# Performance work log

Measured on AMD Instinct MI355X. Metric: run time of the kernel, lower is better.

Reference implementation:

```python
import jax, jax.numpy as jnp
import numpy as np

T = 32.0                       # softmax temperature
THRESH = float(np.cos(np.pi * 40.0 / 180.0))  # cos(degree), degree=40
NEG_INF = -9.0e15


def setup_inputs() -> dict:
    key = jax.random.key(0)
    ks = jax.random.split(key, 11)
    B, C, D_IMG, D_ATT, H_ATT, H = 2048, 1000, 2048, 312, 128, 128
    def rn(k, shape, scale=1.0):
        return jax.random.normal(k, shape, dtype=jnp.float32) * scale
    return {
        "image_feats": rn(ks[0], (B, D_IMG)),
        "img_proto":   rn(ks[1], (C, D_IMG)),
        "attributes":  rn(ks[2], (C, D_ATT)),
        "unused":      0,
        # parameters
        "att_g":   rn(ks[3], (D_ATT, H_ATT), 0.05),
        "slim_w":  rn(ks[4], (D_IMG, D_ATT), 0.02),   # proto_slim weight (transposed torch layout)
        "slim_b":  rn(ks[5], (D_ATT,), 0.02),
        "img_w":   rn(ks[6], (D_IMG, H), 0.02),
        "proto_w": rn(ks[7], (2 * D_ATT, H), 0.02),   # att_dim + proto_red_dim = 624
        "proto_b": rn(ks[8], (1, H), 0.02),
        "fc_w":    rn(ks[9], (H, 1), 0.05),
        "fc_b":    rn(ks[10], (1,), 0.05),
    }


def reference(image_feats, img_proto, attributes, unused,
              att_g, slim_w, slim_b, img_w, proto_w, proto_b, fc_w, fc_b):
    # proto_slim: [C, D_img] -> [C, att_dim]
    proto_red = img_proto @ slim_w + slim_b

    # --- get_attention: cosine similarity among attribute projections ---
    g = attributes @ att_g                                   # [C, att_hC] (g == h in original)
    gn = g / jnp.clip(jnp.linalg.norm(g, axis=1, keepdims=True), 1e-12)
    sim = gn @ gn.T                                          # [C, C] cosine similarity
    raw = jnp.where(sim > THRESH, sim, NEG_INF)              # threshold mask
    attn = jax.nn.softmax(raw * T, axis=1)                   # [C, C]

    # --- propagate prototypes ---
    att_outs = attn @ attributes                             # [C, att_dim]
    img_proto_outs = attn @ proto_red                        # [C, att_dim]
    outs = jnp.concatenate([att_outs, img_proto_outs], axis=1)  # [C, 2*att_dim]

    # --- relation MLP (broadcast instead of materialized expand+matmul) ---
    img_h = image_feats @ img_w                              # [B, H]
    proto_h = outs @ proto_w                                 # [C, H]
    hidden = jax.nn.relu(img_h[:, None, :] + proto_h[None, :, :] + proto_b)  # [B, C, H]
    outputs = hidden @ fc_w + fc_b                           # [B, C, 1]
    return outputs[..., 0]                                   # [B, C]
```

## Files before the change

### kernel.cpp

```cpp
#include <hip/hip_runtime.h>

typedef unsigned short ushort_t;
typedef __bf16 bf16x8 __attribute__((ext_vector_type(8)));
typedef float f32x4 __attribute__((ext_vector_type(4)));
typedef float f32x2 __attribute__((ext_vector_type(2)));
typedef ushort_t us4 __attribute__((ext_vector_type(4)));

#define T_SOFT 32.0f
#define THRESH 0.76604444311897803f
#define SW 1048

__device__ __forceinline__ ushort_t f2bf(float f) {
  union { float f; unsigned u; } x; x.f = f;
  unsigned r = (x.u + 0x7fffu + ((x.u >> 16) & 1u)) >> 16;
  return (ushort_t)r;
}
__device__ __forceinline__ float bf2f(ushort_t h) {
  union { unsigned u; float f; } x; x.u = ((unsigned)h) << 16; return x.f;
}

__device__ __forceinline__ us4 pack4(float4 x) {
  union { unsigned u[2]; us4 h; } r;
  union { float4 f; unsigned u[4]; } a;
  a.f = x;
  r.u[0] = __builtin_amdgcn_perm(a.u[1] + 0x8000u, a.u[0] + 0x8000u, 0x07060302u);
  r.u[1] = __builtin_amdgcn_perm(a.u[3] + 0x8000u, a.u[2] + 0x8000u, 0x07060302u);
  return r.h;
}

__global__ __launch_bounds__(256) void tr3_k(const float* __restrict__ s0, ushort_t* __restrict__ d0,
                                             const float* __restrict__ s1, ushort_t* __restrict__ d1,
                                             const float* __restrict__ s2, ushort_t* __restrict__ d2,
                                             const float* __restrict__ attributes, ushort_t* __restrict__ poutN,
                                             ushort_t* __restrict__ gn_bf, float* __restrict__ zero_base) {
  int b = blockIdx.x, tid = threadIdx.x;
  if (b >= 976) {
    if (b < 1288) {
      int t = (b - 976) * 256 + tid;
      int row = t / 78, c4 = (t - row * 78) * 4;
      us4 v = {0, 0, 0, 0};
      if (row < 1000) v = pack4(*reinterpret_cast<const float4*>(attributes + (size_t)row * 312 + c4));
      *reinterpret_cast<us4*>(poutN + (size_t)row * 640 + c4) = v;
    } else if (b < 1432) {
      int t = (b - 1288) * 256 + tid;
      float4* zp = reinterpret_cast<float4*>(zero_base) + (size_t)t * 4;
      float4 z = make_float4(0.f, 0.f, 0.f, 0.f);
      zp[0] = z; zp[1] = z; zp[2] = z; zp[3] = z;
    } else {
      us4 z = {0, 0, 0, 0};
      *reinterpret_cast<us4*>(gn_bf + 1000 * 128 + tid * 4) = z;
    }
    return;
  }
  __shared__ float tl[32][33];
  const float* src; ushort_t* dst; int R, C, Cw, Rpad, local, ctiles;
  if (b < 640)       { src = s0; dst = d0; R = 2048; C = 312; Cw = 320; Rpad = 2048; local = b;       ctiles = 10; }
  else if (b < 896)  { src = s1; dst = d1; R = 2048; C = 128; Cw = 128; Rpad = 2048; local = b - 640; ctiles = 4;  }
  else               { src = s2; dst = d2; R = 624;  C = 128; Cw = 128; Rpad = 640;  local = b - 896; ctiles = 4;  }
  int rt = local / ctiles, ct = local - rt * ctiles;
  int r0 = rt * 32, c0 = ct * 32;
  #pragma unroll
  for (int p = 0; p < 4; ++p) {
    int idx = p * 256 + tid;
    int rr = idx >> 5, cc = idx & 31;
    float v = 0.f;
    if (r0 + rr < R && c0 + cc < C) v = src[(size_t)(r0 + rr) * C + (c0 + cc)];
    tl[cc][rr] = v;
  }
  __syncthreads();
  int cc = tid >> 3, rq = tid & 7;
  if (c0 + cc < Cw) {
    us4 o;
    o[0] = f2bf(tl[cc][rq * 4 + 0]);
    o[1] = f2bf(tl[cc][rq * 4 + 1]);
    o[2] = f2bf(tl[cc][rq * 4 + 2]);
    o[3] = f2bf(tl[cc][rq * 4 + 3]);
    *reinterpret_cast<us4*>(dst + (size_t)(c0 + cc) * Rpad + r0 + rq * 4) = o;
  }
}

__device__ __forceinline__ void gemm_imgh(const float* __restrict__ A, const ushort_t* __restrict__ BT,
                                          float* __restrict__ C, int r0, int k0,
                                          ushort_t* __restrict__ As, ushort_t* __restrict__ Bs, int tid) {
  const int SA = 72;
  int lane = tid & 63, wv = tid >> 6;
  int l15 = lane & 15, quad = lane >> 4;
  int arow = tid >> 4, akq = tid & 15;
  int brow = tid >> 3, bkq = tid & 7;
  const float* agp[8];
  #pragma unroll
  for (int p = 0; p < 8; ++p) agp[p] = A + (size_t)(r0 + arow + p * 16) * 2048 + k0 + akq * 4;
  const ushort_t* bgp[4];
  #pragma unroll
  for (int p = 0; p < 4; ++p) bgp[p] = BT + (size_t)(brow + p * 32) * 2048 + k0 + bkq * 8;

  float4 ap[8]; bf16x8 bp[4];
  #pragma unroll
  for (int p = 0; p < 8; ++p) ap[p] = *reinterpret_cast<const float4*>(agp[p]);
  #pragma unroll
  for (int p = 0; p < 4; ++p) bp[p] = *reinterpret_cast<const bf16x8*>(bgp[p]);

  f32x4 acc[2][8];
  #pragma unroll
  for (int i = 0; i < 2; ++i)
    #pragma unroll
    for (int j = 0; j < 8; ++j) acc[i][j] = f32x4{0.f, 0.f, 0.f, 0.f};

  for (int s = 0; s < 4; ++s) {
    if (s) __syncthreads();
    #pragma unroll
    for (int p = 0; p < 8; ++p)
      *reinterpret_cast<us4*>(As + (arow + p * 16) * SA + akq * 4) = pack4(ap[p]);
    #pragma unroll
    for (int p = 0; p < 4; ++p)
      *reinterpret_cast<bf16x8*>(Bs + (brow + p * 32) * SA + bkq * 8) = bp[p];
    if (s + 1 < 4) {
      #pragma unroll
      for (int p = 0; p < 8; ++p) ap[p] = *reinterpret_cast<const float4*>(agp[p] + 64);
      #pragma unroll
      for (int p = 0; p < 4; ++p) bp[p] = *reinterpret_cast<const bf16x8*>(bgp[p] + 64);
      #pragma unroll
      for (int p = 0; p < 8; ++p) agp[p] += 64;
      #pragma unroll
      for (int p = 0; p < 4; ++p) bgp[p] += 64;
    }
    __syncthreads();
    #pragma unroll
    for (int kh = 0; kh < 2; ++kh) {
      bf16x8 af[2];
      #pragma unroll
      for (int pi = 0; pi < 2; ++pi)
        af[pi] = *reinterpret_cast<bf16x8*>(As + ((wv * 2 + pi) * 16 + l15) * SA + kh * 32 + quad * 8);
      #pragma unroll
      for (int ct = 0; ct < 8; ++ct) {
        bf16x8 bfr = *reinterpret_cast<bf16x8*>(Bs + (ct * 16 + l15) * SA + kh * 32 + quad * 8);
        acc[0][ct] = __builtin_amdgcn_mfma_f32_16x16x32_bf16(af[0], bfr, acc[0][ct], 0, 0, 0);
        acc[1][ct] = __builtin_amdgcn_mfma_f32_16x16x32_bf16(af[1], bfr, acc[1][ct], 0, 0, 0);
      }
    }
  }
  #pragma unroll
  for (int pi = 0; pi < 2; ++pi)
    #pragma unroll
    for (int ct = 0; ct < 8; ++ct) {
      int col = ct * 16 + l15;
      #pragma unroll
      for (int r = 0; r < 4; ++r) {
        int row = r0 + (wv * 2 + pi) * 16 + quad * 4 + r;
        atomicAdd(&C[(size_t)row * 128 + col], acc[pi][ct][r]);
      }
    }
}

__device__ __forceinline__ void gemm_proto(const float* __restrict__ A, const ushort_t* __restrict__ BT,
                                           float* __restrict__ pacc2, int r0, int c0, int k0,
                                           ushort_t* __restrict__ As, ushort_t* __restrict__ Bs, int tid) {
  const int SA = 72;
  int lane = tid & 63, wv = tid >> 6;
  int l15 = lane & 15, quad = lane >> 4;
  int arow = tid >> 4, akq = tid & 15;
  int brow = tid >> 3, bkq = tid & 7;
  const float* agp[8];
  #pragma unroll
  for (int p = 0; p < 8; ++p) {
    int r = r0 + arow + p * 16; if (r >= 1000) r = 999;
    agp[p] = A + (size_t)r * 2048 + k0 + akq * 4;
  }
  const ushort_t* bgp[4];
  #pragma unroll
  for (int p = 0; p < 4; ++p) {
    int n = c0 + brow + p * 32; if (n >= 320) n = 319;
    bgp[p] = BT + (size_t)n * 2048 + k0 + bkq * 8;
  }
  float4 ap[8]; bf16x8 bp[4];
  #pragma unroll
  for (int p = 0; p < 8; ++p) ap[p] = *reinterpret_cast<const float4*>(agp[p]);
  #pragma unroll
  for (int p = 0; p < 4; ++p) bp[p] = *reinterpret_cast<const bf16x8*>(bgp[p]);

  f32x4 acc[2][8];
  #pragma unroll
  for (int i = 0; i < 2; ++i)
    #pragma unroll
    for (int j = 0; j < 8; ++j) acc[i][j] = f32x4{0.f, 0.f, 0.f, 0.f};

  for (int s = 0; s < 4; ++s) {
    if (s) __syncthreads();
    #pragma unroll
    for (int p = 0; p < 8; ++p)
      *reinterpret_cast<us4*>(As + (arow + p * 16) * SA + akq * 4) = pack4(ap[p]);
    #pragma unroll
    for (int p = 0; p < 4; ++p)
      *reinterpret_cast<bf16x8*>(Bs + (brow + p * 32) * SA + bkq * 8) = bp[p];
    if (s + 1 < 4) {
      #pragma unroll
      for (int p = 0; p < 8; ++p) ap[p] = *reinterpret_cast<const float4*>(agp[p] + 64);
      #pragma unroll
      for (int p = 0; p < 4; ++p) bp[p] = *reinterpret_cast<const bf16x8*>(bgp[p] + 64);
      #pragma unroll
      for (int p = 0; p < 8; ++p) agp[p] += 64;
      #pragma unroll
      for (int p = 0; p < 4; ++p) bgp[p] += 64;
    }
    __syncthreads();
    #pragma unroll
    for (int kh = 0; kh < 2; ++kh) {
      bf16x8 af[2];
      #pragma unroll
      for (int pi = 0; pi < 2; ++pi)
        af[pi] = *reinterpret_cast<bf16x8*>(As + ((wv * 2 + pi) * 16 + l15) * SA + kh * 32 + quad * 8);
      #pragma unroll
      for (int ct = 0; ct < 8; ++ct) {
        bf16x8 bfr = *reinterpret_cast<bf16x8*>(Bs + (ct * 16 + l15) * SA + kh * 32 + quad * 8);
        acc[0][ct] = __builtin_amdgcn_mfma_f32_16x16x32_bf16(af[0], bfr, acc[0][ct], 0, 0, 0);
        acc[1][ct] = __builtin_amdgcn_mfma_f32_16x16x32_bf16(af[1], bfr, acc[1][ct], 0, 0, 0);
      }
    }
  }
  #pragma unroll
  for (int pi = 0; pi < 2; ++pi)
    #pragma unroll
    for (int ct = 0; ct < 8; ++ct) {
      int col = c0 + ct * 16 + l15;
      if (col < 320) {
        #pragma unroll
        for (int r = 0; r < 4; ++r) {
          int row = r0 + (wv * 2 + pi) * 16 + quad * 4 + r;
          atomicAdd(&pacc2[(size_t)row * 320 + col], acc[pi][ct][r]);
        }
      }
    }
}

__global__ __launch_bounds__(256) void mega_k(
    const float* __restrict__ attributes, const float* __restrict__ att_g,
    ushort_t* __restrict__ gn_bf,
    const float* __restrict__ img_proto, const ushort_t* __restrict__ slimT,
    const float* __restrict__ image_feats, const ushort_t* __restrict__ imgwT,
    float* __restrict__ img_h, float* __restrict__ pacc2) {
  __shared__ ushort_t As[128 * 72];
  __shared__ ushort_t Bs[128 * 72];
  int b = blockIdx.x, tid = threadIdx.x;
  if (b < 125) {
    __shared__ float a_lds[8][316];
    __shared__ float red2[8][2];
    int h = tid & 127;
    int c0 = b * 8;
    for (int idx = tid; idx < 8 * 312; idx += 256) {
      int r = idx / 312;
      int k = idx - r * 312;
      a_lds[r][k] = attributes[(c0 + r) * 312 + k];
    }
    __syncthreads();
    float acc[8] = {0.f,0.f,0.f,0.f,0.f,0.f,0.f,0.f};
    for (int k = 0; k < 312; k += 4) {
      float w0 = att_g[(k + 0) * 128 + h];
      float w1 = att_g[(k + 1) * 128 + h];
      float w2 = att_g[(k + 2) * 128 + h];
      float w3 = att_g[(k + 3) * 128 + h];
      #pragma unroll
      for (int r = 0; r < 8; ++r) {
        float4 a4 = *reinterpret_cast<const float4*>(&a_lds[r][k]);
        acc[r] += a4.x * w0 + a4.y * w1 + a4.z * w2 + a4.w * w3;
      }
    }
    int lane = tid & 63, wvid = (tid >> 6) & 1;
    #pragma unroll
    for (int r = 0; r < 8; ++r) {
      float v = acc[r] * acc[r];
      #pragma unroll
      for (int off = 32; off > 0; off >>= 1) v += __shfl_xor(v, off, 64);
      if (lane == 0) red2[r][wvid] = v;
    }
    __syncthreads();
    #pragma unroll
    for (int r = 0; r < 8; ++r) {
      float nrm = fmaxf(sqrtf(red2[r][0] + red2[r][1]), 1e-12f);
      gn_bf[(c0 + r) * 128 + h] = f2bf(acc[r] / nrm);
    }
    return;
  }
  b -= 125;
  if (b < 128) {
    int tile = b >> 3, kc = b & 7;
    gemm_imgh(image_feats, imgwT, img_h, tile * 128, kc * 256, As, Bs, tid);
  } else {
    b -= 128;
    int tile = b >> 3, kc = b & 7;
    int rb = tile / 3, cb = tile - rb * 3;
    gemm_proto(img_proto, slimT, pacc2, rb * 128, cb * 128, kc * 256, As, Bs, tid);
  }
}

__global__ __launch_bounds__(256) void conv_k(const float* __restrict__ pacc2, ushort_t* __restrict__ poutN) {
  int t = blockIdx.x * 256 + threadIdx.x;
  int row = t / 82, m = (t - row * 82) * 4;
  us4 v = {0, 0, 0, 0};
  if (m < 320) v = pack4(*reinterpret_cast<const float4*>(pacc2 + (size_t)row * 320 + m));
  *reinterpret_cast<us4*>(poutN + (size_t)row * 640 + 312 + m) = v;
}

__global__ __launch_bounds__(256) void g_k(const ushort_t* __restrict__ protowT, const ushort_t* __restrict__ poutN,
                                           const float* __restrict__ proto_w, const float* __restrict__ slim_b,
                                           const float* __restrict__ proto_b,
                                           ushort_t* __restrict__ GT, float* __restrict__ biasG) {
  int b = blockIdx.x, tid = threadIdx.x;
  if (b >= 8) {
    int h = tid & 127;
    float acc = proto_b[h];
    for (int n = 0; n < 312; n += 4) {
      acc += slim_b[n + 0] * proto_w[(size_t)(312 + n) * 128 + h];
      acc += slim_b[n + 1] * proto_w[(size_t)(313 + n) * 128 + h];
      acc += slim_b[n + 2] * proto_w[(size_t)(314 + n) * 128 + h];
      acc += slim_b[n + 3] * proto_w[(size_t)(315 + n) * 128 + h];
    }
    if (tid < 128) biasG[h] = acc;
    return;
  }
  const int SA = 72;
  __shared__ ushort_t As[128 * 72];
  __shared__ ushort_t Bs[128 * 72];
  int lane = tid & 63, wv = tid >> 6;
  int l15 = lane & 15, quad = lane >> 4;
  int hrow = tid >> 3, hkq = tid & 7;
  size_t j0 = (size_t)b * 128;
  const ushort_t* agp[4];
  const ushort_t* bgp[4];
  #pragma unroll
  for (int p = 0; p < 4; ++p) {
    agp[p] = protowT + (size_t)(hrow + p * 32) * 640 + hkq * 8;
    bgp[p] = poutN + (j0 + hrow + p * 32) * 640 + hkq * 8;
  }
  bf16x8 ar[4], br[4];
  #pragma unroll
  for (int p = 0; p < 4; ++p) { ar[p] = *reinterpret_cast<const bf16x8*>(agp[p]); br[p] = *reinterpret_cast<const bf16x8*>(bgp[p]); }

  f32x4 acc[2][8];
  #pragma unroll
  for (int i = 0; i < 2; ++i)
    #pragma unroll
    for (int j = 0; j < 8; ++j) acc[i][j] = f32x4{0.f, 0.f, 0.f, 0.f};

  for (int s = 0; s < 10; ++s) {
    if (s) __syncthreads();
    #pragma unroll
    for (int p = 0; p < 4; ++p) {
      *reinterpret_cast<bf16x8*>(As + (hrow + p * 32) * SA + hkq * 8) = ar[p];
      *reinterpret_cast<bf16x8*>(Bs + (hrow + p * 32) * SA + hkq * 8) = br[p];
    }
    if (s + 1 < 10) {
      #pragma unroll
      for (int p = 0; p < 4; ++p) {
        ar[p] = *reinterpret_cast<const bf16x8*>(agp[p] + 64);
        br[p] = *reinterpret_cast<const bf16x8*>(bgp[p] + 64);
        agp[p] += 64; bgp[p] += 64;
      }
    }
    __syncthreads();
    #pragma unroll
    for (int kh = 0; kh < 2; ++kh) {
      bf16x8 af[2];
      #pragma unroll
      for (int pi = 0; pi < 2; ++pi)
        af[pi] = *reinterpret_cast<bf16x8*>(As + ((wv * 2 + pi) * 16 + l15) * SA + kh * 32 + quad * 8);
      #pragma unroll
      for (int ct = 0; ct < 8; ++ct) {
        bf16x8 bfr = *reinterpret_cast<bf16x8*>(Bs + (ct * 16 + l15) * SA + kh * 32 + quad * 8);
        acc[0][ct] = __builtin_amdgcn_mfma_f32_16x16x32_bf16(af[0], bfr, acc[0][ct], 0, 0, 0);
        acc[1][ct] = __builtin_amdgcn_mfma_f32_16x16x32_bf16(af[1], bfr, acc[1][ct], 0, 0, 0);
      }
    }
  }
  #pragma unroll
  for (int pi = 0; pi < 2; ++pi)
    #pragma unroll
    for (int ct = 0; ct < 8; ++ct) {
      int col = ct * 16 + l15;
      #pragma unroll
      for (int r = 0; r < 4; ++r) {
        int row = (wv * 2 + pi) * 16 + quad * 4 + r;
        GT[(size_t)row * 1024 + j0 + col] = f2bf(acc[pi][ct][r]);
      }
    }
}

__global__ __launch_bounds__(256) void attn5_k(
    const ushort_t* __restrict__ gn_bf, const ushort_t* __restrict__ GT,
    const float* __restrict__ biasG, float* __restrict__ ph) {
  __shared__ ushort_t W[16 * SW];
  __shared__ float rsum[16];
  __shared__ int flags[63];
  int tid = threadIdx.x;
  int i0 = blockIdx.x * 16;
  int lane = tid & 63, wv = tid >> 6;
  int l15 = lane & 15, quad = lane >> 4;
  if (tid < 63) flags[tid] = 0;
  if (tid >= 64 && tid < 80) rsum[tid - 64] = 0.f;
  W[(tid >> 4) * SW + 1008 + (tid & 15)] = 0;
  __syncthreads();

  const ushort_t* abase = gn_bf + (size_t)(i0 + l15) * 128 + quad * 8;
  bf16x8 af0 = *reinterpret_cast<const bf16x8*>(abase);
  bf16x8 af1 = *reinterpret_cast<const bf16x8*>(abase + 32);
  bf16x8 af2 = *reinterpret_cast<const bf16x8*>(abase + 64);
  bf16x8 af3 = *reinterpret_cast<const bf16x8*>(abase + 96);
  float rs[4] = {0.f, 0.f, 0.f, 0.f};
  for (int jt = wv; jt < 63; jt += 4) {
    const ushort_t* bbase = gn_bf + (size_t)(jt * 16 + l15) * 128 + quad * 8;
    f32x4 d = {0.f, 0.f, 0.f, 0.f};
    d = __builtin_amdgcn_mfma_f32_16x16x32_bf16(af0, *reinterpret_cast<const bf16x8*>(bbase),      d, 0, 0, 0);
    d = __builtin_amdgcn_mfma_f32_16x16x32_bf16(af1, *reinterpret_cast<const bf16x8*>(bbase + 32), d, 0, 0, 0);
    d = __builtin_amdgcn_mfma_f32_16x16x32_bf16(af2, *reinterpret_cast<const bf16x8*>(bbase + 64), d, 0, 0, 0);
    d = __builtin_amdgcn_mfma_f32_16x16x32_bf16(af3, *reinterpret_cast<const bf16x8*>(bbase + 96), d, 0, 0, 0);
    int hot = 0;
    #pragma unroll
    for (int r = 0; r < 4; ++r) {
      float w = 0.f;
      if (d[r] > THRESH) { w = __expf(T_SOFT * (d[r] - 1.0f)); hot = 1; }
      ushort_t wb = f2bf(w);
      W[(quad * 4 + r) * SW + jt * 16 + l15] = wb;
      rs[r] += bf2f(wb);
    }
    if (hot) flags[jt] = 1;
  }
  #pragma unroll
  for (int r = 0; r < 4; ++r) {
    float v = rs[r];
    v += __shfl_xor(v, 1, 64); v += __shfl_xor(v, 2, 64);
    v += __shfl_xor(v, 4, 64); v += __shfl_xor(v, 8, 64);
    if (l15 == 0) atomicAdd(&rsum[quad * 4 + r], v);
  }
  __syncthreads();

  f32x4 acc2[2];
  acc2[0] = f32x4{0.f, 0.f, 0.f, 0.f};
  acc2[1] = f32x4{0.f, 0.f, 0.f, 0.f};
  for (int s = 0; s < 32; ++s) {
    int f = flags[2 * s] | ((2 * s + 1 < 63) ? flags[2 * s + 1] : 0);
    if (!f) continue;
    bf16x8 a = *reinterpret_cast<bf16x8*>(W + l15 * SW + s * 32 + quad * 8);
    #pragma unroll
    for (int t = 0; t < 2; ++t) {
      int h = (wv * 2 + t) * 16 + l15;
      bf16x8 bfr = *reinterpret_cast<const bf16x8*>(GT + (size_t)h * 1024 + s * 32 + quad * 8);
      acc2[t] = __builtin_amdgcn_mfma_f32_16x16x32_bf16(a, bfr, acc2[t], 0, 0, 0);
    }
  }
  #pragma unroll
  for (int t = 0; t < 2; ++t) {
    int h = (wv * 2 + t) * 16 + l15;
    float bg = biasG[h];
    #pragma unroll
    for (int r = 0; r < 4; ++r) {
      int row = quad * 4 + r;
      int gi = i0 + row;
      float inv = 1.f / fmaxf(rsum[row], 1e-30f);
      if (gi < 1000) ph[(size_t)gi * 128 + h] = acc2[t][r] * inv + bg;
    }
  }
}

__global__ __launch_bounds__(512) void final_k(
    const float* __restrict__ img_h, const float* __restrict__ ph,
    const float* __restrict__ fc_w, const float* __restrict__ fc_b,
    float* __restrict__ out) {
  __shared__ float ih[128][132];
  __shared__ float ps[64][132];
  __shared__ float ws_[128];
  int tid = threadIdx.x;
  int b0 = blockIdx.x * 128;
  int c0 = blockIdx.y * 64;
  for (int idx = tid; idx < 4096; idx += 512) {
    int row = idx >> 5, c4 = (idx & 31) * 4;
    float4 v = *reinterpret_cast<const float4*>(img_h + (size_t)(b0 + row) * 128 + c4);
    *reinterpret_cast<float4*>(&ih[row][c4]) = v;
  }
  for (int idx = tid; idx < 2048; idx += 512) {
    int row = idx >> 5, c4 = (idx & 31) * 4;
    int c = c0 + row;
    float4 v = make_float4(0.f, 0.f, 0.f, 0.f);
    if (c < 1000) v = *reinterpret_cast<const float4*>(ph + (size_t)c * 128 + c4);
    *reinterpret_cast<float4*>(&ps[row][c4]) = v;
  }
  if (tid < 128) ws_[tid] = fc_w[tid];
  __syncthreads();
  int tx = tid & 15, ty = tid >> 4;
  f32x2 acc[4][4] = {};
  const f32x2 zero2 = {0.f, 0.f};
  for (int h = 0; h < 128; h += 4) {
    float4 w4 = *reinterpret_cast<float4*>(&ws_[h]);
    f32x2 wlo = {w4.x, w4.y}, whi = {w4.z, w4.w};
    float4 a4[4], p4[4];
    #pragma unroll
    for (int i = 0; i < 4; ++i) a4[i] = *reinterpret_cast<float4*>(&ih[ty * 4 + i][h]);
    #pragma unroll
    for (int j = 0; j < 4; ++j) p4[j] = *reinterpret_cast<float4*>(&ps[tx * 4 + j][h]);
    #pragma unroll
    for (int i = 0; i < 4; ++i) {
      f32x2 alo = {a4[i].x, a4[i].y}, ahi = {a4[i].z, a4[i].w};
      #pragma unroll
      for (int j = 0; j < 4; ++j) {
        f32x2 plo = {p4[j].x, p4[j].y}, phi = {p4[j].z, p4[j].w};
        f32x2 t0 = __builtin_elementwise_max(alo + plo, zero2);
        f32x2 t1 = __builtin_elementwise_max(ahi + phi, zero2);
        acc[i][j] = acc[i][j] + t0 * wlo;
        acc[i][j] = acc[i][j] + t1 * whi;
      }
    }
  }
  float fb = fc_b[0];
  #pragma unroll
  for (int i = 0; i < 4; ++i) {
    int b = b0 + ty * 4 + i;
    int c = c0 + tx * 4;
    if (c < 1000) {
      float4 v = make_float4(acc[i][0].x + acc[i][0].y + fb, acc[i][1].x + acc[i][1].y + fb,
                             acc[i][2].x + acc[i][2].y + fb, acc[i][3].x + acc[i][3].y + fb);
      *reinterpret_cast<float4*>(out + (size_t)b * 1000 + c) = v;
    }
  }
}

extern "C" void kernel_launch(void* const* d_in, const int* in_sizes, int n_in,
                              void* d_out, int out_size, void* d_ws, size_t ws_size,
                              hipStream_t stream) {
  const float* image_feats = (const float*)d_in[0];
  const float* img_proto   = (const float*)d_in[1];
  const float* attributes  = (const float*)d_in[2];
  const float* att_g   = (const float*)d_in[4];
  const float* slim_w  = (const float*)d_in[5];
  const float* slim_b  = (const float*)d_in[6];
  const float* img_w   = (const float*)d_in[7];
  const float* proto_w = (const float*)d_in[8];
  const float* proto_b = (const float*)d_in[9];
  const float* fc_w    = (const float*)d_in[10];
  const float* fc_b    = (const float*)d_in[11];
  float* out = (float*)d_out;

  char* ws = (char*)d_ws;
  size_t o = 0;
  auto alloc = [&](size_t bytes) { size_t r = o; o += (bytes + 255) & ~(size_t)255; return r; };
  ushort_t* imgwT   = (ushort_t*)(ws + alloc(128ull * 2048 * 2));
  ushort_t* slimT   = (ushort_t*)(ws + alloc(320ull * 2048 * 2));
  ushort_t* protowT = (ushort_t*)(ws + alloc(128ull * 640 * 2));
  ushort_t* gn_bf   = (ushort_t*)(ws + alloc(1008ull * 128 * 2));
  ushort_t* poutN   = (ushort_t*)(ws + alloc(1024ull * 640 * 2));
  ushort_t* GT      = (ushort_t*)(ws + alloc(128ull * 1024 * 2));
  float* biasG     = (float*)(ws + alloc(128ull * 4));
  float* img_h     = (float*)(ws + alloc(2048ull * 128 * 4));
  float* pacc2     = (float*)(ws + alloc(1024ull * 320 * 4));
  float* ph        = (float*)(ws + alloc(1000ull * 128 * 4));

  tr3_k<<<1433, 256, 0, stream>>>(slim_w, slimT, img_w, imgwT, proto_w, protowT,
                                  attributes, poutN, gn_bf, img_h);

  mega_k<<<445, 256, 0, stream>>>(attributes, att_g, gn_bf,
                                  img_proto, slimT,
                                  image_feats, imgwT, img_h, pacc2);

  conv_k<<<328, 256, 0, stream>>>(pacc2, poutN);

  g_k<<<9, 256, 0, stream>>>(protowT, poutN, proto_w, slim_b, proto_b, GT, biasG);

  attn5_k<<<63, 256, 0, stream>>>(gn_bf, GT, biasG, ph);

  final_k<<<dim3(16, 16), 512, 0, stream>>>(img_h, ph, fc_w, fc_b, out);
}
```

Before: 179.3 us.

## Reassociate proto path to fold slim_w into proto_w and drop atomics

```diff
diff --git a/kernel.cpp b/kernel.cpp
--- a/kernel.cpp
+++ b/kernel.cpp
@@ -28,36 +28,56 @@
   return r.h;
 }
 
-__global__ __launch_bounds__(256) void tr3_k(const float* __restrict__ s0, ushort_t* __restrict__ d0,
-                                             const float* __restrict__ s1, ushort_t* __restrict__ d1,
-                                             const float* __restrict__ s2, ushort_t* __restrict__ d2,
-                                             const float* __restrict__ attributes, ushort_t* __restrict__ poutN,
-                                             ushort_t* __restrict__ gn_bf, float* __restrict__ zero_base) {
+__global__ __launch_bounds__(256) void tr3_k(const float* __restrict__ img_w, ushort_t* __restrict__ imgwT,
+                                             const float* __restrict__ proto_w, ushort_t* __restrict__ protowT,
+                                             const float* __restrict__ slim_w, ushort_t* __restrict__ slim_bf,
+                                             const float* __restrict__ attributes, ushort_t* __restrict__ attr_bf,
+                                             ushort_t* __restrict__ gn_bf,
+                                             const float* __restrict__ slim_b, const float* __restrict__ proto_b,
+                                             float* __restrict__ biasG) {
   int b = blockIdx.x, tid = threadIdx.x;
-  if (b >= 976) {
-    if (b < 1288) {
-      int t = (b - 976) * 256 + tid;
-      int row = t / 78, c4 = (t - row * 78) * 4;
-      us4 v = {0, 0, 0, 0};
-      if (row < 1000) v = pack4(*reinterpret_cast<const float4*>(attributes + (size_t)row * 312 + c4));
-      *reinterpret_cast<us4*>(poutN + (size_t)row * 640 + c4) = v;
-    } else if (b < 1432) {
-      int t = (b - 1288) * 256 + tid;
-      float4* zp = reinterpret_cast<float4*>(zero_base) + (size_t)t * 4;
-      float4 z = make_float4(0.f, 0.f, 0.f, 0.f);
-      zp[0] = z; zp[1] = z; zp[2] = z; zp[3] = z;
-    } else {
+  if (b >= 336) {
+    if (b < 496) {
+      int t = (b - 336) * 256 + tid;
+      int row = t / 20, c0 = (t - row * 20) * 16;
+      #pragma unroll
+      for (int g = 0; g < 4; ++g) {
+        int c4 = c0 + g * 4;
+        us4 v = {0, 0, 0, 0};
+        if (c4 < 312) v = pack4(*reinterpret_cast<const float4*>(slim_w + (size_t)row * 312 + c4));
+        *reinterpret_cast<us4*>(slim_bf + (size_t)row * 320 + c4) = v;
+      }
+    } else if (b < 576) {
+      int t = (b - 496) * 256 + tid;
+      int row = t / 20, c0 = (t - row * 20) * 16;
+      #pragma unroll
+      for (int g = 0; g < 4; ++g) {
+        int c4 = c0 + g * 4;
+        us4 v = {0, 0, 0, 0};
+        if (row < 1000 && c4 < 312) v = pack4(*reinterpret_cast<const float4*>(attributes + (size_t)row * 312 + c4));
+        *reinterpret_cast<us4*>(attr_bf + (size_t)row * 320 + c4) = v;
+      }
+    } else if (b == 576) {
       us4 z = {0, 0, 0, 0};
       *reinterpret_cast<us4*>(gn_bf + 1000 * 128 + tid * 4) = z;
+    } else {
+      int h = tid & 127;
+      float acc = proto_b[h];
+      for (int n = 0; n < 312; n += 4) {
+        acc += slim_b[n + 0] * proto_w[(size_t)(312 + n) * 128 + h];
+        acc += slim_b[n + 1] * proto_w[(size_t)(313 + n) * 128 + h];
+        acc += slim_b[n + 2] * proto_w[(size_t)(314 + n) * 128 + h];
+        acc += slim_b[n + 3] * proto_w[(size_t)(315 + n) * 128 + h];
+      }
+      if (tid < 128) biasG[h] = acc;
     }
     return;
   }
   __shared__ float tl[32][33];
-  const float* src; ushort_t* dst; int R, C, Cw, Rpad, local, ctiles;
-  if (b < 640)       { src = s0; dst = d0; R = 2048; C = 312; Cw = 320; Rpad = 2048; local = b;       ctiles = 10; }
-  else if (b < 896)  { src = s1; dst = d1; R = 2048; C = 128; Cw = 128; Rpad = 2048; local = b - 640; ctiles = 4;  }
-  else               { src = s2; dst = d2; R = 624;  C = 128; Cw = 128; Rpad = 640;  local = b - 896; ctiles = 4;  }
-  int rt = local / ctiles, ct = local - rt * ctiles;
+  const float* src; ushort_t* dst; int R, C, Rpad, local;
+  if (b < 256) { src = img_w;   dst = imgwT;   R = 2048; C = 128; Rpad = 2048; local = b;       }
+  else         { src = proto_w; dst = protowT; R = 624;  C = 128; Rpad = 640;  local = b - 256; }
+  int rt = local >> 2, ct = local & 3;
   int r0 = rt * 32, c0 = ct * 32;
   #pragma unroll
   for (int p = 0; p < 4; ++p) {
@@ -69,18 +89,16 @@
   }
   __syncthreads();
   int cc = tid >> 3, rq = tid & 7;
-  if (c0 + cc < Cw) {
-    us4 o;
-    o[0] = f2bf(tl[cc][rq * 4 + 0]);
-    o[1] = f2bf(tl[cc][rq * 4 + 1]);
-    o[2] = f2bf(tl[cc][rq * 4 + 2]);
-    o[3] = f2bf(tl[cc][rq * 4 + 3]);
-    *reinterpret_cast<us4*>(dst + (size_t)(c0 + cc) * Rpad + r0 + rq * 4) = o;
-  }
+  us4 o;
+  o[0] = f2bf(tl[cc][rq * 4 + 0]);
+  o[1] = f2bf(tl[cc][rq * 4 + 1]);
+  o[2] = f2bf(tl[cc][rq * 4 + 2]);
+  o[3] = f2bf(tl[cc][rq * 4 + 3]);
+  *reinterpret_cast<us4*>(dst + (size_t)(c0 + cc) * Rpad + r0 + rq * 4) = o;
 }
 
 __device__ __forceinline__ void gemm_imgh(const float* __restrict__ A, const ushort_t* __restrict__ BT,
-                                          float* __restrict__ C, int r0, int k0,
+                                          float* __restrict__ Cp, int r0, int k0,
                                           ushort_t* __restrict__ As, ushort_t* __restrict__ Bs, int tid) {
   const int SA = 72;
   int lane = tid & 63, wv = tid >> 6;
@@ -147,60 +165,41 @@
       #pragma unroll
       for (int r = 0; r < 4; ++r) {
         int row = r0 + (wv * 2 + pi) * 16 + quad * 4 + r;
-        atomicAdd(&C[(size_t)row * 128 + col], acc[pi][ct][r]);
-      }
-    }
-}
-
-__device__ __forceinline__ void gemm_proto(const float* __restrict__ A, const ushort_t* __restrict__ BT,
-                                           float* __restrict__ pacc2, int r0, int c0, int k0,
-                                           ushort_t* __restrict__ As, ushort_t* __restrict__ Bs, int tid) {
+        Cp[(size_t)row * 128 + col] = acc[pi][ct][r];
+      }
+    }
+}
+
+__device__ __forceinline__ void gemm_bb(const ushort_t* __restrict__ A, int sa,
+                                        const ushort_t* __restrict__ B, int sb,
+                                        int nsteps, ushort_t* __restrict__ As, ushort_t* __restrict__ Bs,
+                                        int tid, f32x4 acc[2][8]) {
   const int SA = 72;
   int lane = tid & 63, wv = tid >> 6;
   int l15 = lane & 15, quad = lane >> 4;
-  int arow = tid >> 4, akq = tid & 15;
-  int brow = tid >> 3, bkq = tid & 7;
-  const float* agp[8];
-  #pragma unroll
-  for (int p = 0; p < 8; ++p) {
-    int r = r0 + arow + p * 16; if (r >= 1000) r = 999;
-    agp[p] = A + (size_t)r * 2048 + k0 + akq * 4;
-  }
-  const ushort_t* bgp[4];
+  int hrow = tid >> 3, hkq = tid & 7;
+  const ushort_t* ap = A + (size_t)hrow * sa + hkq * 8;
+  const ushort_t* bp = B + (size_t)hrow * sb + hkq * 8;
+  bf16x8 ar[4], br[4];
   #pragma unroll
   for (int p = 0; p < 4; ++p) {
-    int n = c0 + brow + p * 32; if (n >= 320) n = 319;
-    bgp[p] = BT + (size_t)n * 2048 + k0 + bkq * 8;
-  }
-  float4 ap[8]; bf16x8 bp[4];
-  #pragma unroll
-  for (int p = 0; p < 8; ++p) ap[p] = *reinterpret_cast<const float4*>(agp[p]);
-  #pragma unroll
-  for (int p = 0; p < 4; ++p) bp[p] = *reinterpret_cast<const bf16x8*>(bgp[p]);
-
-  f32x4 acc[2][8];
-  #pragma unroll
-  for (int i = 0; i < 2; ++i)
-    #pragma unroll
-    for (int j = 0; j < 8; ++j) acc[i][j] = f32x4{0.f, 0.f, 0.f, 0.f};
-
-  for (int s = 0; s < 4; ++s) {
+    ar[p] = *reinterpret_cast<const bf16x8*>(ap + (size_t)p * 32 * sa);
+    br[p] = *reinterpret_cast<const bf16x8*>(bp + (size_t)p * 32 * sb);
+  }
+  for (int s = 0; s < nsteps; ++s) {
     if (s) __syncthreads();
     #pragma unroll
-    for (int p = 0; p < 8; ++p)
-      *reinterpret_cast<us4*>(As + (arow + p * 16) * SA + akq * 4) = pack4(ap[p]);
-    #pragma unroll
-    for (int p = 0; p < 4; ++p)
-      *reinterpret_cast<bf16x8*>(Bs + (brow + p * 32) * SA + bkq * 8) = bp[p];
-    if (s + 1 < 4) {
-      #pragma unroll
-      for (int p = 0; p < 8; ++p) ap[p] = *reinterpret_cast<const float4*>(agp[p] + 64);
-      #pragma unroll
-      for (int p = 0; p < 4; ++p) bp[p] = *reinterpret_cast<const bf16x8*>(bgp[p] + 64);
-      #pragma unroll
-      for (int p = 0; p < 8; ++p) agp[p] += 64;
-      #pragma unroll
-      for (int p = 0; p < 4; ++p) bgp[p] += 64;
+    for (int p = 0; p < 4; ++p) {
+      *reinterpret_cast<bf16x8*>(As + (hrow + p * 32) * SA + hkq * 8) = ar[p];
+      *reinterpret_cast<bf16x8*>(Bs + (hrow + p * 32) * SA + hkq * 8) = br[p];
+    }
+    if (s + 1 < nsteps) {
+      ap += 64; bp += 64;
+      #pragma unroll
+      for (int p = 0; p < 4; ++p) {
+        ar[p] = *reinterpret_cast<const bf16x8*>(ap + (size_t)p * 32 * sa);
+        br[p] = *reinterpret_cast<const bf16x8*>(bp + (size_t)p * 32 * sb);
+      }
     }
     __syncthreads();
     #pragma unroll
@@ -217,27 +216,68 @@
       }
     }
   }
-  #pragma unroll
-  for (int pi = 0; pi < 2; ++pi)
-    #pragma unroll
-    for (int ct = 0; ct < 8; ++ct) {
-      int col = c0 + ct * 16 + l15;
-      if (col < 320) {
-        #pragma unroll
-        for (int r = 0; r < 4; ++r) {
-          int row = r0 + (wv * 2 + pi) * 16 + quad * 4 + r;
-          atomicAdd(&pacc2[(size_t)row * 320 + col], acc[pi][ct][r]);
-        }
-      }
-    }
+}
+
+__device__ __forceinline__ void gemm_b32(const ushort_t* __restrict__ A, int sa,
+                                         const float* __restrict__ Bsrc, int sb, int brow0, int browmax,
+                                         int nsteps, ushort_t* __restrict__ As, ushort_t* __restrict__ Bs,
+                                         int tid, f32x4 acc[2][8]) {
+  const int SA = 72;
+  int lane = tid & 63, wv = tid >> 6;
+  int l15 = lane & 15, quad = lane >> 4;
+  int hrow = tid >> 3, hkq = tid & 7;
+  int frow = tid >> 4, fkq = tid & 15;
+  const ushort_t* ap = A + (size_t)hrow * sa + hkq * 8;
+  const float* bgp[8];
+  #pragma unroll
+  for (int p = 0; p < 8; ++p) {
+    int r = brow0 + frow + p * 16; if (r > browmax) r = browmax;
+    bgp[p] = Bsrc + (size_t)r * sb + fkq * 4;
+  }
+  bf16x8 ar[4]; float4 brf[8];
+  #pragma unroll
+  for (int p = 0; p < 4; ++p) ar[p] = *reinterpret_cast<const bf16x8*>(ap + (size_t)p * 32 * sa);
+  #pragma unroll
+  for (int p = 0; p < 8; ++p) brf[p] = *reinterpret_cast<const float4*>(bgp[p]);
+  for (int s = 0; s < nsteps; ++s) {
+    if (s) __syncthreads();
+    #pragma unroll
+    for (int p = 0; p < 4; ++p)
+      *reinterpret_cast<bf16x8*>(As + (hrow + p * 32) * SA + hkq * 8) = ar[p];
+    #pragma unroll
+    for (int p = 0; p < 8; ++p)
+      *reinterpret_cast<us4*>(Bs + (frow + p * 16) * SA + fkq * 4) = pack4(brf[p]);
+    if (s + 1 < nsteps) {
+      ap += 64;
+      #pragma unroll
+      for (int p = 0; p < 4; ++p) ar[p] = *reinterpret_cast<const bf16x8*>(ap + (size_t)p * 32 * sa);
+      #pragma unroll
+      for (int p = 0; p < 8; ++p) { bgp[p] += 64; brf[p] = *reinterpret_cast<const float4*>(bgp[p]); }
+    }
+    __syncthreads();
+    #pragma unroll
+    for (int kh = 0; kh < 2; ++kh) {
+      bf16x8 af[2];
+      #pragma unroll
+      for (int pi = 0; pi < 2; ++pi)
+        af[pi] = *reinterpret_cast<bf16x8*>(As + ((wv * 2 + pi) * 16 + l15) * SA + kh * 32 + quad * 8);
+      #pragma unroll
+      for (int ct = 0; ct < 8; ++ct) {
+        bf16x8 bfr = *reinterpret_cast<bf16x8*>(Bs + (ct * 16 + l15) * SA + kh * 32 + quad * 8);
+        acc[0][ct] = __builtin_amdgcn_mfma_f32_16x16x32_bf16(af[0], bfr, acc[0][ct], 0, 0, 0);
+        acc[1][ct] = __builtin_amdgcn_mfma_f32_16x16x32_bf16(af[1], bfr, acc[1][ct], 0, 0, 0);
+      }
+    }
+  }
 }
 
 __global__ __launch_bounds__(256) void mega_k(
     const float* __restrict__ attributes, const float* __restrict__ att_g,
     ushort_t* __restrict__ gn_bf,
-    const float* __restrict__ img_proto, const ushort_t* __restrict__ slimT,
     const float* __restrict__ image_feats, const ushort_t* __restrict__ imgwT,
-    float* __restrict__ img_h, float* __restrict__ pacc2) {
+    float* __restrict__ ihp,
+    const ushort_t* __restrict__ protowT, const ushort_t* __restrict__ slim_bf,
+    ushort_t* __restrict__ M2T) {
   __shared__ ushort_t As[128 * 72];
   __shared__ ushort_t Bs[128 * 72];
   int b = blockIdx.x, tid = threadIdx.x;
@@ -253,6 +293,7 @@
     }
     __syncthreads();
     float acc[8] = {0.f,0.f,0.f,0.f,0.f,0.f,0.f,0.f};
+    #pragma unroll 2
     for (int k = 0; k < 312; k += 4) {
       float w0 = att_g[(k + 0) * 128 + h];
       float w1 = att_g[(k + 1) * 128 + h];
@@ -283,110 +324,108 @@
   b -= 125;
   if (b < 128) {
     int tile = b >> 3, kc = b & 7;
-    gemm_imgh(image_feats, imgwT, img_h, tile * 128, kc * 256, As, Bs, tid);
-  } else {
-    b -= 128;
-    int tile = b >> 3, kc = b & 7;
-    int rb = tile / 3, cb = tile - rb * 3;
-    gemm_proto(img_proto, slimT, pacc2, rb * 128, cb * 128, kc * 256, As, Bs, tid);
-  }
-}
-
-__global__ __launch_bounds__(256) void conv_k(const float* __restrict__ pacc2, ushort_t* __restrict__ poutN) {
-  int t = blockIdx.x * 256 + threadIdx.x;
-  int row = t / 82, m = (t - row * 82) * 4;
-  us4 v = {0, 0, 0, 0};
-  if (m < 320) v = pack4(*reinterpret_cast<const float4*>(pacc2 + (size_t)row * 320 + m));
-  *reinterpret_cast<us4*>(poutN + (size_t)row * 640 + 312 + m) = v;
-}
-
-__global__ __launch_bounds__(256) void g_k(const ushort_t* __restrict__ protowT, const ushort_t* __restrict__ poutN,
-                                           const float* __restrict__ proto_w, const float* __restrict__ slim_b,
-                                           const float* __restrict__ proto_b,
-                                           ushort_t* __restrict__ GT, float* __restrict__ biasG) {
-  int b = blockIdx.x, tid = threadIdx.x;
-  if (b >= 8) {
-    int h = tid & 127;
-    float acc = proto_b[h];
-    for (int n = 0; n < 312; n += 4) {
-      acc += slim_b[n + 0] * proto_w[(size_t)(312 + n) * 128 + h];
-      acc += slim_b[n + 1] * proto_w[(size_t)(313 + n) * 128 + h];
-      acc += slim_b[n + 2] * proto_w[(size_t)(314 + n) * 128 + h];
-      acc += slim_b[n + 3] * proto_w[(size_t)(315 + n) * 128 + h];
-    }
-    if (tid < 128) biasG[h] = acc;
+    gemm_imgh(image_feats, imgwT, ihp + (size_t)kc * 2048 * 128, tile * 128, kc * 256, As, Bs, tid);
     return;
   }
-  const int SA = 72;
+  b -= 128;
+  int c0 = b * 128;
+  f32x4 acc[2][8];
+  #pragma unroll
+  for (int i = 0; i < 2; ++i)
+    #pragma unroll
+    for (int j = 0; j < 8; ++j) acc[i][j] = f32x4{0.f, 0.f, 0.f, 0.f};
+  gemm_bb(protowT + 312, 640, slim_bf + (size_t)c0 * 320, 320, 5, As, Bs, tid, acc);
+  int lane = tid & 63, wv = tid >> 6;
+  int l15 = lane & 15, quad = lane >> 4;
+  #pragma unroll
+  for (int pi = 0; pi < 2; ++pi)
+    #pragma unroll
+    for (int ct = 0; ct < 8; ++ct) {
+      int col = c0 + ct * 16 + l15;
+      #pragma unroll
+      for (int r = 0; r < 4; ++r) {
+        int row = (wv * 2 + pi) * 16 + quad * 4 + r;
+        M2T[(size_t)row * 2048 + col] = f2bf(acc[pi][ct][r]);
+      }
+    }
+}
+
+__global__ __launch_bounds__(256) void k3_k(
+    const float* __restrict__ ihp, float* __restrict__ img_h,
+    const ushort_t* __restrict__ protowT, const ushort_t* __restrict__ M2T,
+    const ushort_t* __restrict__ attr_bf, const float* __restrict__ img_proto,
+    float* __restrict__ GT_part) {
   __shared__ ushort_t As[128 * 72];
   __shared__ ushort_t Bs[128 * 72];
+  int b = blockIdx.x, tid = threadIdx.x;
+  if (b < 64) {
+    int t = b * 256 + tid;
+    size_t base = (size_t)t * 16;
+    #pragma unroll
+    for (int g = 0; g < 4; ++g) {
+      float4 s = *reinterpret_cast<const float4*>(ihp + base + g * 4);
+      #pragma unroll
+      for (int c = 1; c < 8; ++c) {
+        float4 v = *reinterpret_cast<const float4*>(ihp + (size_t)c * 262144 + base + g * 4);
+        s.x += v.x; s.y += v.y; s.z += v.z; s.w += v.w;
+      }
+      *reinterpret_cast<float4*>(img_h + base + g * 4) = s;
+    }
+    return;
+  }
+  int q = b - 64;
+  int jt = q / 5, ch = q - jt * 5;
+  int j0 = jt * 128;
+  f32x4 acc[2][8];
+  #pragma unroll
+  for (int i = 0; i < 2; ++i)
+    #pragma unroll
+    for (int j = 0; j < 8; ++j) acc[i][j] = f32x4{0.f, 0.f, 0.f, 0.f};
+  if (ch == 0) {
+    gemm_bb(protowT, 640, attr_bf + (size_t)j0 * 320, 320, 5, As, Bs, tid, acc);
+  } else {
+    int k0 = (ch - 1) * 512;
+    gemm_b32(M2T + k0, 2048, img_proto + k0, 2048, j0, 999, 8, As, Bs, tid, acc);
+  }
   int lane = tid & 63, wv = tid >> 6;
   int l15 = lane & 15, quad = lane >> 4;
-  int hrow = tid >> 3, hkq = tid & 7;
-  size_t j0 = (size_t)b * 128;
-  const ushort_t* agp[4];
-  const ushort_t* bgp[4];
-  #pragma unroll
-  for (int p = 0; p < 4; ++p) {
-    agp[p] = protowT + (size_t)(hrow + p * 32) * 640 + hkq * 8;
-    bgp[p] = poutN + (j0 + hrow + p * 32) * 640 + hkq * 8;
-  }
-  bf16x8 ar[4], br[4];
-  #pragma unroll
-  for (int p = 0; p < 4; ++p) { ar[p] = *reinterpret_cast<const bf16x8*>(agp[p]); br[p] = *reinterpret_cast<const bf16x8*>(bgp[p]); }
-
-  f32x4 acc[2][8];
-  #pragma unroll
-  for (int i = 0; i < 2; ++i)
-    #pragma unroll
-    for (int j = 0; j < 8; ++j) acc[i][j] = f32x4{0.f, 0.f, 0.f, 0.f};
-
-  for (int s = 0; s < 10; ++s) {
-    if (s) __syncthreads();
-    #pragma unroll
-    for (int p = 0; p < 4; ++p) {
-      *reinterpret_cast<bf16x8*>(As + (hrow + p * 32) * SA + hkq * 8) = ar[p];
-      *reinterpret_cast<bf16x8*>(Bs + (hrow + p * 32) * SA + hkq * 8) = br[p];
-    }
-    if (s + 1 < 10) {
-      #pragma unroll
-      for (int p = 0; p < 4; ++p) {
-        ar[p] = *reinterpret_cast<const bf16x8*>(agp[p] + 64);
-        br[p] = *reinterpret_cast<const bf16x8*>(bgp[p] + 64);
-        agp[p] += 64; bgp[p] += 64;
-      }
-    }
-    __syncthreads();
-    #pragma unroll
-    for (int kh = 0; kh < 2; ++kh) {
-      bf16x8 af[2];
-      #pragma unroll
-      for (int pi = 0; pi < 2; ++pi)
-        af[pi] = *reinterpret_cast<bf16x8*>(As + ((wv * 2 + pi) * 16 + l15) * SA + kh * 32 + quad * 8);
-      #pragma unroll
-      for (int ct = 0; ct < 8; ++ct) {
-        bf16x8 bfr = *reinterpret_cast<bf16x8*>(Bs + (ct * 16 + l15) * SA + kh * 32 + quad * 8);
-        acc[0][ct] = __builtin_amdgcn_mfma_f32_16x16x32_bf16(af[0], bfr, acc[0][ct], 0, 0, 0);
-        acc[1][ct] = __builtin_amdgcn_mfma_f32_16x16x32_bf16(af[1], bfr, acc[1][ct], 0, 0, 0);
-      }
-    }
-  }
+  float* dst = GT_part + (size_t)ch * 128 * 1024;
   #pragma unroll
   for (int pi = 0; pi < 2; ++pi)
     #pragma unroll
     for (int ct = 0; ct < 8; ++ct) {
-      int col = ct * 16 + l15;
+      int col = j0 + ct * 16 + l15;
       #pragma unroll
       for (int r = 0; r < 4; ++r) {
         int row = (wv * 2 + pi) * 16 + quad * 4 + r;
-        GT[(size_t)row * 1024 + j0 + col] = f2bf(acc[pi][ct][r]);
-      }
-    }
+        dst[(size_t)row * 1024 + col] = acc[pi][ct][r];
+      }
+    }
+}
+
+__global__ __launch_bounds__(256) void k4_k(const float* __restrict__ GT_part,
+                                            const float* __restrict__ biasG,
+                                            ushort_t* __restrict__ GT) {
+  int t = blockIdx.x * 256 + threadIdx.x;
+  size_t base = (size_t)t * 16;
+  int row = (int)(base >> 10);
+  float bg = biasG[row];
+  #pragma unroll
+  for (int g = 0; g < 4; ++g) {
+    float4 s = *reinterpret_cast<const float4*>(GT_part + base + g * 4);
+    #pragma unroll
+    for (int c = 1; c < 5; ++c) {
+      float4 v = *reinterpret_cast<const float4*>(GT_part + (size_t)c * 131072 + base + g * 4);
+      s.x += v.x; s.y += v.y; s.z += v.z; s.w += v.w;
+    }
+    s.x += bg; s.y += bg; s.z += bg; s.w += bg;
+    *reinterpret_cast<us4*>(GT + base + g * 4) = pack4(s);
+  }
 }
 
 __global__ __launch_bounds__(256) void attn5_k(
     const ushort_t* __restrict__ gn_bf, const ushort_t* __restrict__ GT,
-    const float* __restrict__ biasG, float* __restrict__ ph) {
+    float* __restrict__ ph) {
   __shared__ ushort_t W[16 * SW];
   __shared__ float rsum[16];
   __shared__ int flags[63];
@@ -449,13 +488,12 @@
   #pragma unroll
   for (int t = 0; t < 2; ++t) {
     int h = (wv * 2 + t) * 16 + l15;
-    float bg = biasG[h];
     #pragma unroll
     for (int r = 0; r < 4; ++r) {
       int row = quad * 4 + r;
       int gi = i0 + row;
       float inv = 1.f / fmaxf(rsum[row], 1e-30f);
-      if (gi < 1000) ph[(size_t)gi * 128 + h] = acc2[t][r] * inv + bg;
+      if (gi < 1000) ph[(size_t)gi * 128 + h] = acc2[t][r] * inv;
     }
   }
 }
@@ -541,28 +579,29 @@
   size_t o = 0;
   auto alloc = [&](size_t bytes) { size_t r = o; o += (bytes + 255) & ~(size_t)255; return r; };
   ushort_t* imgwT   = (ushort_t*)(ws + alloc(128ull * 2048 * 2));
-  ushort_t* slimT   = (ushort_t*)(ws + alloc(320ull * 2048 * 2));
   ushort_t* protowT = (ushort_t*)(ws + alloc(128ull * 640 * 2));
+  ushort_t* slim_bf = (ushort_t*)(ws + alloc(2048ull * 320 * 2));
+  ushort_t* attr_bf = (ushort_t*)(ws + alloc(1024ull * 320 * 2));
   ushort_t* gn_bf   = (ushort_t*)(ws + alloc(1008ull * 128 * 2));
-  ushort_t* poutN   = (ushort_t*)(ws + alloc(1024ull * 640 * 2));
+  ushort_t* M2T     = (ushort_t*)(ws + alloc(128ull * 2048 * 2));
   ushort_t* GT      = (ushort_t*)(ws + alloc(128ull * 1024 * 2));
   float* biasG     = (float*)(ws + alloc(128ull * 4));
+  float* ihp       = (float*)(ws + alloc(8ull * 2048 * 128 * 4));
+  float* GT_part   = (float*)(ws + alloc(5ull * 128 * 1024 * 4));
   float* img_h     = (float*)(ws + alloc(2048ull * 128 * 4));
-  float* pacc2     = (float*)(ws + alloc(1024ull * 320 * 4));
   float* ph        = (float*)(ws + alloc(1000ull * 128 * 4));
 
-  tr3_k<<<1433, 256, 0, stream>>>(slim_w, slimT, img_w, imgwT, proto_w, protowT,
-                                  attributes, poutN, gn_bf, img_h);
-
-  mega_k<<<445, 256, 0, stream>>>(attributes, att_g, gn_bf,
-                                  img_proto, slimT,
-                                  image_feats, imgwT, img_h, pacc2);
-
-  conv_k<<<328, 256, 0, stream>>>(pacc2, poutN);
-
-  g_k<<<9, 256, 0, stream>>>(protowT, poutN, proto_w, slim_b, proto_b, GT, biasG);
-
-  attn5_k<<<63, 256, 0, stream>>>(gn_bf, GT, biasG, ph);
+  tr3_k<<<578, 256, 0, stream>>>(img_w, imgwT, proto_w, protowT, slim_w, slim_bf,
+                                 attributes, attr_bf, gn_bf, slim_b, proto_b, biasG);
+
+  mega_k<<<269, 256, 0, stream>>>(attributes, att_g, gn_bf,
+                                  image_feats, imgwT, ihp, protowT, slim_bf, M2T);
+
+  k3_k<<<104, 256, 0, stream>>>(ihp, img_h, protowT, M2T, attr_bf, img_proto, GT_part);
+
+  k4_k<<<32, 256, 0, stream>>>(GT_part, biasG, GT);
+
+  attn5_k<<<63, 256, 0, stream>>>(gn_bf, GT, ph);
 
   final_k<<<dim3(16, 16), 512, 0, stream>>>(img_h, ph, fc_w, fc_b, out);
 }
```

After: 169.9 us. 5.3% less time.
